# Performance work log

Measured on AMD Instinct MI355X. Metric: run time of the kernel, lower is better.

## Reference

```python
import jax, jax.numpy as jnp
import numpy as np

N = 10000        # num_nodes
D = 256          # num_attrs
AVG_DEG = 32
K = N // 2       # known nodes
ALPHA = 0.5
BETA = 0.5


def setup_inputs() -> dict:
    rng = np.random.default_rng(0)
    # random graph -> symmetric adjacency (duplicate edges coalesce by summation,
    # matching torch_geometric coalescing of edge weights)
    src = rng.integers(0, N, size=N * AVG_DEG)
    dst = rng.integers(0, N, size=N * AVG_DEG)
    A = np.zeros((N, N), dtype=np.float32)
    np.add.at(A, (src, dst), 1.0)
    np.add.at(A, (dst, src), 1.0)
    # symmetric normalized Laplacian: L = I - D^{-1/2} A D^{-1/2}
    deg = A.sum(axis=1)
    dinv = np.where(deg > 0, 1.0 / np.sqrt(np.maximum(deg, 1e-12)), 0.0).astype(np.float32)
    L = np.eye(N, dtype=np.float32) - (dinv[:, None] * A * dinv[None, :])

    raw_x = rng.standard_normal((N, D)).astype(np.float32)
    know = np.sort(rng.choice(N, size=K, replace=False)).astype(np.int64)
    mean = raw_x[know].mean(axis=0)                 # is_binary=False path
    out_k_init = (raw_x[know] - mean).astype(np.float32)  # std = 1
    x = np.zeros((N, D), dtype=np.float32)
    x[know] = raw_x[know]                           # nn.Parameter init

    theta = np.float32((1.0 - 1.0 / N) * (1.0 / ALPHA - 1.0))
    eta = np.float32((1.0 / BETA - 1.0) / ALPHA)
    return {
        "x": jnp.asarray(x),
        "L": jnp.asarray(L),
        "mean": jnp.asarray(mean),
        "out_k_init": jnp.asarray(out_k_init),
        "know_mask": jnp.asarray(know),
        "theta": jnp.asarray(theta),
        "eta": jnp.asarray(eta),
    }


def reference(x, L, mean, out_k_init, know_mask, theta, eta):
    n = x.shape[0]
    xn = x - mean  # std = 1
    # dirichlet loss: sum_f x_f^T L x_f == sum(xn * (L @ xn))
    dirichlet = jnp.sum(xn * (L @ xn))
    # avg_L = n/(n-1) I - 1/(n-1) 11^T  ->  quadratic form in closed form
    col = xn.sum(axis=0)  # [D]
    avg = (n / (n - 1)) * jnp.sum(xn * xn) - (1.0 / (n - 1)) * jnp.sum(col * col)
    # MSE with reduction='sum'
    recon = jnp.sum((xn[know_mask] - out_k_init) ** 2)
    return -(dirichlet + eta * recon + theta * avg)
```

## Files before the change

kernel.cpp:

```cpp
#include <hip/hip_runtime.h>


#define NN    10000
#define DD    256
#define PREPB 157
#define RECB  256
#define SBLK  1250
#define QCAP  2048

typedef float  f32x4 __attribute__((ext_vector_type(4)));
typedef short  s16x8 __attribute__((ext_vector_type(8)));
typedef short  s16x4 __attribute__((ext_vector_type(4)));

__device__ __forceinline__ unsigned short f2bf(float f) {
    union { float f; unsigned u; } c; c.f = f;
    unsigned u = c.u;
    u += 0x7fffu + ((u >> 16) & 1u);
    return (unsigned short)(u >> 16);
}
__device__ __forceinline__ float bfr(unsigned short h) {
    union { unsigned u; float f; } c; c.u = ((unsigned)h) << 16; return c.f;
}

__global__ __launch_bounds__(256) void prep_kernel(const float* __restrict__ x,
                                                   const float* __restrict__ mean,
                                                   const float* __restrict__ oki,
                                                   const int* __restrict__ know,
                                                   int K,
                                                   unsigned short* __restrict__ xnR,
                                                   float* __restrict__ csbuf,
                                                   float* __restrict__ ssbuf,
                                                   float* __restrict__ rbuf) {
    __shared__ __align__(16) unsigned short xs[64][264];
    __shared__ float red[8];
    const int t  = threadIdx.x;
    const int bb = blockIdx.x;
    if (bb < PREPB) {
        const int i0 = bb * 64;
        float ss = 0.f;
#pragma unroll
        for (int p = 0; p < 16; ++p) {
            const int li  = p * 256 + t;
            const int row = li >> 6;
            const int c4  = li & 63;
            const int gi  = i0 + row;
            f32x4 v = {0.f, 0.f, 0.f, 0.f};
            if (gi < NN) {
                const f32x4 xv = *(const f32x4*)(x + (size_t)gi * DD + c4 * 4);
                const f32x4 mv = *(const f32x4*)(mean + c4 * 4);
                v[0] = xv[0] - mv[0]; v[1] = xv[1] - mv[1];
                v[2] = xv[2] - mv[2]; v[3] = xv[3] - mv[3];
                ss += v[0]*v[0] + v[1]*v[1] + v[2]*v[2] + v[3]*v[3];
            }
            unsigned short h[4];
            h[0] = f2bf(v[0]); h[1] = f2bf(v[1]); h[2] = f2bf(v[2]); h[3] = f2bf(v[3]);
            *(s16x4*)&xs[row][c4 * 4] = *(const s16x4*)h;
        }
#pragma unroll
        for (int off = 32; off > 0; off >>= 1) ss += __shfl_xor(ss, off);
        if ((t & 63) == 0) red[t >> 6] = ss;
        __syncthreads();
        if (t == 0) ssbuf[bb] = red[0] + red[1] + red[2] + red[3];
        float css = 0.f;
        for (int ii = 0; ii < 64; ++ii) css += bfr(xs[ii][t]);
        csbuf[(size_t)bb * 256 + t] = css;
#pragma unroll
        for (int p = 0; p < 8; ++p) {
            const int row  = p * 8 + (t >> 5);
            const int colb = (t & 31) * 8;
            const int i = i0 + row;
            if (i < NN)
                *(s16x8*)(xnR + (size_t)i * DD + colb) = *(const s16x8*)&xs[row][colb];
        }
    } else {
        const int rb = bb - PREPB;
        const int w  = t >> 6, l = t & 63;
        const f32x4 mv = *(const f32x4*)(mean + l * 4);
        float s = 0.f;
        for (int r = rb * 4 + w; r < K; r += RECB * 4) {
            const int idx = know[r];
            const f32x4 xv = *(const f32x4*)(x   + (size_t)idx * DD + l * 4);
            const f32x4 ov = *(const f32x4*)(oki + (size_t)r   * DD + l * 4);
            const float d0 = xv[0] - mv[0] - ov[0];
            const float d1 = xv[1] - mv[1] - ov[1];
            const float d2 = xv[2] - mv[2] - ov[2];
            const float d3 = xv[3] - mv[3] - ov[3];
            s += d0*d0 + d1*d1 + d2*d2 + d3*d3;
        }
#pragma unroll
        for (int off = 32; off > 0; off >>= 1) s += __shfl_xor(s, off);
        if (l == 0) red[4 + w] = s;
        __syncthreads();
        if (t == 0) rbuf[rb] = red[4] + red[5] + red[6] + red[7];
    }
}

__global__ __launch_bounds__(256) void sdot_kernel(const float* __restrict__ L,
                                                   const unsigned short* __restrict__ xnR,
                                                   float* __restrict__ part) {
    __shared__ unsigned qidx[QCAP];
    __shared__ float    qval[QCAP];
    __shared__ __align__(16) unsigned short irw[8][264];
    __shared__ unsigned qcnt;
    __shared__ float red[4];
    const int t = threadIdx.x;
    const int b = blockIdx.x;
    const int r0 = 8 * b;
    if (t == 0) qcnt = 0;
    {
        const int sr = t >> 5, sc = (t & 31) * 8;
        *(s16x8*)&irw[sr][sc] = *(const s16x8*)(xnR + (size_t)(r0 + sr) * DD + sc);
    }
    __syncthreads();

    const int lenA = (NN - r0 + 15) >> 4;
    const int lenB = (NN - r0 - 4 + 15) >> 4;
    const int pre1 = lenA;            const int pre2 = 2 * lenA;
    const int pre3 = 3 * lenA;        const int pre4 = 4 * lenA;
    const int pre5 = pre4 + lenB;     const int pre6 = pre4 + 2 * lenB;
    const int pre7 = pre4 + 3 * lenB;
    const int ntot = pre4 + 4 * lenB;

#define DECODE(g_)                                                             \
    int rr_ = 0, base_ = 0;                                                    \
    if ((g_) >= pre1) { rr_ = 1; base_ = pre1; }                               \
    if ((g_) >= pre2) { rr_ = 2; base_ = pre2; }                               \
    if ((g_) >= pre3) { rr_ = 3; base_ = pre3; }                               \
    if ((g_) >= pre4) { rr_ = 4; base_ = pre4; }                               \
    if ((g_) >= pre5) { rr_ = 5; base_ = pre5; }                               \
    if ((g_) >= pre6) { rr_ = 6; base_ = pre6; }                               \
    if ((g_) >= pre7) { rr_ = 7; base_ = pre7; }                               \
    const int i_ = r0 + rr_;                                                   \
    const int c_ = (i_ & ~3) + (((g_) - base_) << 4);

#define ISSUE(V0_, V1_, V2_, V3_, g_) {                                        \
    if ((g_) < ntot) {                                                         \
        DECODE(g_)                                                             \
        const float* p_ = L + (size_t)i_ * NN + c_;                            \
        if (c_ + 16 <= NN) {                                                   \
            V0_ = *(const f32x4*)p_;        V1_ = *(const f32x4*)(p_ + 4);     \
            V2_ = *(const f32x4*)(p_ + 8);  V3_ = *(const f32x4*)(p_ + 12);    \
        } else {                                                               \
            _Pragma("unroll") for (int e_ = 0; e_ < 4; ++e_) {                 \
                V0_[e_] = (c_ + e_      < NN) ? p_[e_]      : 0.f;             \
                V1_[e_] = (c_ + e_ + 4  < NN) ? p_[e_ + 4]  : 0.f;             \
                V2_[e_] = (c_ + e_ + 8  < NN) ? p_[e_ + 8]  : 0.f;             \
                V3_[e_] = (c_ + e_ + 12 < NN) ? p_[e_ + 12] : 0.f;             \
            } } } }

#define PROC(V0_, V1_, V2_, V3_, g_) {                                         \
    if ((g_) < ntot) {                                                         \
        unsigned orv_ = 0u;                                                    \
        _Pragma("unroll") for (int e_ = 0; e_ < 4; ++e_)                       \
            orv_ |= __float_as_uint(V0_[e_]) | __float_as_uint(V1_[e_])        \
                  | __float_as_uint(V2_[e_]) | __float_as_uint(V3_[e_]);       \
        if (orv_ != 0u) {                                                      \
            DECODE(g_)                                                         \
            _Pragma("unroll") for (int e_ = 0; e_ < 16; ++e_) {                \
                const float v_ = (e_ < 4) ? V0_[e_] : (e_ < 8) ? V1_[e_ - 4]   \
                               : (e_ < 12) ? V2_[e_ - 8] : V3_[e_ - 12];       \
                const int j_ = c_ + e_;                                        \
                if (v_ != 0.f && j_ >= i_ && j_ < NN) {                        \
                    const unsigned s_ = atomicAdd(&qcnt, 1u);                  \
                    if (s_ < QCAP) {                                           \
                        qidx[s_] = ((unsigned)rr_ << 14) | (unsigned)j_;       \
                        qval[s_] = (j_ == i_) ? v_ : 2.f * v_;                 \
                    } } } } } }

    f32x4 A0, A1, A2, A3, B0, B1, B2, B3, C0, C1, C2, C3;
    int g = t;
    ISSUE(A0, A1, A2, A3, g)
    ISSUE(B0, B1, B2, B3, g + 256)
    ISSUE(C0, C1, C2, C3, g + 512)
    while (g < ntot) {
        PROC (A0, A1, A2, A3, g)
        ISSUE(A0, A1, A2, A3, g + 768)
        PROC (B0, B1, B2, B3, g + 256)
        ISSUE(B0, B1, B2, B3, g + 1024)
        PROC (C0, C1, C2, C3, g + 512)
        ISSUE(C0, C1, C2, C3, g + 1280)
        g += 768;
    }
#undef ISSUE
#undef PROC
#undef DECODE
    __syncthreads();
    const unsigned cnt = (qcnt < QCAP) ? qcnt : QCAP;

    const int grp = t >> 3;
    const int ln  = t & 7;
    const int cb  = ln * 32;
    float acc = 0.f;
    for (unsigned e = grp; e < cnt; e += 64) {
        const unsigned eB   = e + 32;
        const bool     hasB = (eB < cnt);
        const unsigned pkA = qidx[e];
        const unsigned pkB = hasB ? qidx[eB] : pkA;
        const int rrA = (int)(pkA >> 14), jA = (int)(pkA & 16383u);
        const int rrB = (int)(pkB >> 14), jB = (int)(pkB & 16383u);
        const unsigned short* pjA = xnR + (size_t)jA * DD + cb;
        const unsigned short* pjB = xnR + (size_t)jB * DD + cb;
        float dA = 0.f, dB = 0.f;
        {
            const s16x8 ja0 = *(const s16x8*)pjA,        ja1 = *(const s16x8*)(pjA + 8);
            const s16x8 jb0 = *(const s16x8*)pjB,        jb1 = *(const s16x8*)(pjB + 8);
            const s16x8 ia0 = *(const s16x8*)&irw[rrA][cb];
            const s16x8 ia1 = *(const s16x8*)&irw[rrA][cb + 8];
            const s16x8 ib0 = *(const s16x8*)&irw[rrB][cb];
            const s16x8 ib1 = *(const s16x8*)&irw[rrB][cb + 8];
#pragma unroll
            for (int k = 0; k < 8; ++k) {
                dA += bfr((unsigned short)ia0[k]) * bfr((unsigned short)ja0[k]);
                dB += bfr((unsigned short)ib0[k]) * bfr((unsigned short)jb0[k]);
            }
#pragma unroll
            for (int k = 0; k < 8; ++k) {
                dA += bfr((unsigned short)ia1[k]) * bfr((unsigned short)ja1[k]);
                dB += bfr((unsigned short)ib1[k]) * bfr((unsigned short)jb1[k]);
            }
        }
        {
            const s16x8 ja2 = *(const s16x8*)(pjA + 16), ja3 = *(const s16x8*)(pjA + 24);
            const s16x8 jb2 = *(const s16x8*)(pjB + 16), jb3 = *(const s16x8*)(pjB + 24);
            const s16x8 ia2 = *(const s16x8*)&irw[rrA][cb + 16];
            const s16x8 ia3 = *(const s16x8*)&irw[rrA][cb + 24];
            const s16x8 ib2 = *(const s16x8*)&irw[rrB][cb + 16];
            const s16x8 ib3 = *(const s16x8*)&irw[rrB][cb + 24];
#pragma unroll
            for (int k = 0; k < 8; ++k) {
                dA += bfr((unsigned short)ia2[k]) * bfr((unsigned short)ja2[k]);
                dB += bfr((unsigned short)ib2[k]) * bfr((unsigned short)jb2[k]);
            }
#pragma unroll
            for (int k = 0; k < 8; ++k) {
                dA += bfr((unsigned short)ia3[k]) * bfr((unsigned short)ja3[k]);
                dB += bfr((unsigned short)ib3[k]) * bfr((unsigned short)jb3[k]);
            }
        }
#pragma unroll
        for (int off = 1; off < 8; off <<= 1) {
            dA += __shfl_xor(dA, off);
            dB += __shfl_xor(dB, off);
        }
        if (ln == 0) {
            acc += qval[e] * dA;
            if (hasB) acc += qval[eB] * dB;
        }
    }
#pragma unroll
    for (int off = 32; off > 0; off >>= 1) acc += __shfl_xor(acc, off);
    if ((t & 63) == 0) red[t >> 6] = acc;
    __syncthreads();
    if (t == 0) part[b] = red[0] + red[1] + red[2] + red[3];
}

__global__ __launch_bounds__(256) void fin_kernel(const float* __restrict__ part,
                                                  const float* __restrict__ csbuf,
                                                  const float* __restrict__ ssbuf,
                                                  const float* __restrict__ rbuf,
                                                  const float* __restrict__ theta,
                                                  const float* __restrict__ eta,
                                                  float* __restrict__ out) {
    __shared__ float red[4][4];
    const int t = threadIdx.x;
    float sp = 0.f;
    for (int i = t; i < SBLK; i += 256) sp += part[i];
    float cs = 0.f;
    for (int bb = 0; bb < PREPB; ++bb) cs += csbuf[(size_t)bb * 256 + t];
    float c2 = cs * cs;
    float ssv = (t < PREPB) ? ssbuf[t] : 0.f;
    float rv  = rbuf[t];
#pragma unroll
    for (int off = 32; off > 0; off >>= 1) {
        sp  += __shfl_xor(sp, off);
        c2  += __shfl_xor(c2, off);
        ssv += __shfl_xor(ssv, off);
        rv  += __shfl_xor(rv, off);
    }
    if ((t & 63) == 0) {
        red[t >> 6][0] = sp; red[t >> 6][1] = c2;
        red[t >> 6][2] = ssv; red[t >> 6][3] = rv;
    }
    __syncthreads();
    if (t == 0) {
        float dir = 0.f, colsq = 0.f, ss = 0.f, rec = 0.f;
#pragma unroll
        for (int w = 0; w < 4; ++w) {
            dir += red[w][0]; colsq += red[w][1];
            ss  += red[w][2]; rec   += red[w][3];
        }
        const float n = (float)NN;
        const float avg = (n / (n - 1.f)) * ss - colsq / (n - 1.f);
        out[0] = -(dir + eta[0] * rec + theta[0] * avg);
    }
}

extern "C" void kernel_launch(void* const* d_in, const int* in_sizes, int n_in,
                              void* d_out, int out_size, void* d_ws, size_t ws_size,
                              hipStream_t stream) {
    const float* x     = (const float*)d_in[0];
    const float* L     = (const float*)d_in[1];
    const float* mean  = (const float*)d_in[2];
    const float* oki   = (const float*)d_in[3];
    const int*   know  = (const int*)d_in[4];
    const float* theta = (const float*)d_in[5];
    const float* eta   = (const float*)d_in[6];
    float* out = (float*)d_out;

    char* ws = (char*)d_ws;
    unsigned short* xnR = (unsigned short*)ws;
    float* part  = (float*)(ws + 6 * 1024 * 1024);
    float* csbuf = (float*)(ws + 7 * 1024 * 1024);
    float* ssbuf = (float*)(ws + 8 * 1024 * 1024);
    float* rbuf  = (float*)(ws + 8 * 1024 * 1024 + 4096);
    const int K = in_sizes[4];

    hipLaunchKernelGGL(prep_kernel, dim3(PREPB + RECB), dim3(256), 0, stream,
                       x, mean, oki, know, K, xnR, csbuf, ssbuf, rbuf);
    hipLaunchKernelGGL(sdot_kernel, dim3(SBLK), dim3(256), 0, stream, L, xnR, part);
    hipLaunchKernelGGL(fin_kernel,  dim3(1),    dim3(256), 0, stream,
                       part, csbuf, ssbuf, rbuf, theta, eta, out);
}
```

Measured before the change: 83.63 us.

## Fuse prep and sparse-dot kernels, drop bf16 copy, pair rows for balance

Merges the prep and sparse-dot passes into one launch, so the sparse-dot blocks no longer wait for a bf16 copy of the centered features. They read fp32 x directly and subtract the mean on the fly. Each block now pairs four rows from the top with four rows from the bottom of the upper triangle, which evens out per-block scan length. This removes a kernel boundary and a write/read of the intermediate, at the cost of reading fp32 gathers (twice the bytes of bf16) in the dot-product phase.

```diff
diff --git a/kernel.cpp b/kernel.cpp
--- a/kernel.cpp
+++ b/kernel.cpp
@@ -7,119 +7,66 @@
 #define RECB  256
 #define SBLK  1250
 #define QCAP  2048
+#define NBLK  (SBLK + PREPB + RECB)
 
 typedef float  f32x4 __attribute__((ext_vector_type(4)));
-typedef short  s16x8 __attribute__((ext_vector_type(8)));
-typedef short  s16x4 __attribute__((ext_vector_type(4)));
-
-__device__ __forceinline__ unsigned short f2bf(float f) {
-    union { float f; unsigned u; } c; c.f = f;
-    unsigned u = c.u;
-    u += 0x7fffu + ((u >> 16) & 1u);
-    return (unsigned short)(u >> 16);
-}
-__device__ __forceinline__ float bfr(unsigned short h) {
-    union { unsigned u; float f; } c; c.u = ((unsigned)h) << 16; return c.f;
-}
-
-__global__ __launch_bounds__(256) void prep_kernel(const float* __restrict__ x,
+
+__global__ __launch_bounds__(256) void mega_kernel(const float* __restrict__ L,
+                                                   const float* __restrict__ x,
                                                    const float* __restrict__ mean,
                                                    const float* __restrict__ oki,
                                                    const int* __restrict__ know,
                                                    int K,
-                                                   unsigned short* __restrict__ xnR,
+                                                   float* __restrict__ part,
                                                    float* __restrict__ csbuf,
                                                    float* __restrict__ ssbuf,
                                                    float* __restrict__ rbuf) {
-    __shared__ __align__(16) unsigned short xs[64][264];
-    __shared__ float red[8];
+    __shared__ __align__(16) char smem[26688];
+    unsigned* qidx = (unsigned*)smem;
+    float*    qval = (float*)(smem + 8192);
+    char*     irw  = smem + 16384;
+    float*    red  = (float*)(smem + 26624);
+    unsigned* qcnt = (unsigned*)(smem + 26640);
+    float*    xsf  = (float*)smem;
+#define XSF(r_, c_) xsf[(r_) * 68 + (c_)]
+#define IRW(rr_, ln_) (irw + (rr_) * 1280 + (ln_) * 80)
+
     const int t  = threadIdx.x;
     const int bb = blockIdx.x;
-    if (bb < PREPB) {
-        const int i0 = bb * 64;
-        float ss = 0.f;
-#pragma unroll
-        for (int p = 0; p < 16; ++p) {
-            const int li  = p * 256 + t;
-            const int row = li >> 6;
-            const int c4  = li & 63;
-            const int gi  = i0 + row;
-            f32x4 v = {0.f, 0.f, 0.f, 0.f};
-            if (gi < NN) {
-                const f32x4 xv = *(const f32x4*)(x + (size_t)gi * DD + c4 * 4);
-                const f32x4 mv = *(const f32x4*)(mean + c4 * 4);
-                v[0] = xv[0] - mv[0]; v[1] = xv[1] - mv[1];
-                v[2] = xv[2] - mv[2]; v[3] = xv[3] - mv[3];
-                ss += v[0]*v[0] + v[1]*v[1] + v[2]*v[2] + v[3]*v[3];
-            }
-            unsigned short h[4];
-            h[0] = f2bf(v[0]); h[1] = f2bf(v[1]); h[2] = f2bf(v[2]); h[3] = f2bf(v[3]);
-            *(s16x4*)&xs[row][c4 * 4] = *(const s16x4*)h;
-        }
-#pragma unroll
-        for (int off = 32; off > 0; off >>= 1) ss += __shfl_xor(ss, off);
-        if ((t & 63) == 0) red[t >> 6] = ss;
-        __syncthreads();
-        if (t == 0) ssbuf[bb] = red[0] + red[1] + red[2] + red[3];
-        float css = 0.f;
-        for (int ii = 0; ii < 64; ++ii) css += bfr(xs[ii][t]);
-        csbuf[(size_t)bb * 256 + t] = css;
-#pragma unroll
-        for (int p = 0; p < 8; ++p) {
-            const int row  = p * 8 + (t >> 5);
-            const int colb = (t & 31) * 8;
-            const int i = i0 + row;
-            if (i < NN)
-                *(s16x8*)(xnR + (size_t)i * DD + colb) = *(const s16x8*)&xs[row][colb];
-        }
-    } else {
-        const int rb = bb - PREPB;
-        const int w  = t >> 6, l = t & 63;
-        const f32x4 mv = *(const f32x4*)(mean + l * 4);
-        float s = 0.f;
-        for (int r = rb * 4 + w; r < K; r += RECB * 4) {
-            const int idx = know[r];
-            const f32x4 xv = *(const f32x4*)(x   + (size_t)idx * DD + l * 4);
-            const f32x4 ov = *(const f32x4*)(oki + (size_t)r   * DD + l * 4);
-            const float d0 = xv[0] - mv[0] - ov[0];
-            const float d1 = xv[1] - mv[1] - ov[1];
-            const float d2 = xv[2] - mv[2] - ov[2];
-            const float d3 = xv[3] - mv[3] - ov[3];
-            s += d0*d0 + d1*d1 + d2*d2 + d3*d3;
-        }
-#pragma unroll
-        for (int off = 32; off > 0; off >>= 1) s += __shfl_xor(s, off);
-        if (l == 0) red[4 + w] = s;
-        __syncthreads();
-        if (t == 0) rbuf[rb] = red[4] + red[5] + red[6] + red[7];
-    }
-}
-
-__global__ __launch_bounds__(256) void sdot_kernel(const float* __restrict__ L,
-                                                   const unsigned short* __restrict__ xnR,
-                                                   float* __restrict__ part) {
-    __shared__ unsigned qidx[QCAP];
-    __shared__ float    qval[QCAP];
-    __shared__ __align__(16) unsigned short irw[8][264];
-    __shared__ unsigned qcnt;
-    __shared__ float red[4];
-    const int t = threadIdx.x;
-    const int b = blockIdx.x;
-    const int r0 = 8 * b;
-    if (t == 0) qcnt = 0;
-    {
-        const int sr = t >> 5, sc = (t & 31) * 8;
-        *(s16x8*)&irw[sr][sc] = *(const s16x8*)(xnR + (size_t)(r0 + sr) * DD + sc);
-    }
-    __syncthreads();
-
-    const int lenA = (NN - r0 + 15) >> 4;
-    const int lenB = (NN - r0 - 4 + 15) >> 4;
-    const int pre1 = lenA;            const int pre2 = 2 * lenA;
-    const int pre3 = 3 * lenA;        const int pre4 = 4 * lenA;
-    const int pre5 = pre4 + lenB;     const int pre6 = pre4 + 2 * lenB;
-    const int pre7 = pre4 + 3 * lenB;
-    const int ntot = pre4 + 4 * lenB;
+
+    if (bb < SBLK) {
+        const int b   = bb;
+        const int ibt = 4 * b;
+        const int ibb = NN - 8 - 4 * b;
+        if (t == 0) *qcnt = 0;
+        {
+            const int sr = t >> 5, q = t & 31;
+            const int si = (sr < 4) ? (ibt + sr) : (ibb + sr);
+            const int c8 = q * 8;
+            const f32x4 xv0 = *(const f32x4*)(x + (size_t)si * DD + c8);
+            const f32x4 xv1 = *(const f32x4*)(x + (size_t)si * DD + c8 + 4);
+            const f32x4 mv0 = *(const f32x4*)(mean + c8);
+            const f32x4 mv1 = *(const f32x4*)(mean + c8 + 4);
+            f32x4 a, c;
+            a[0]=xv0[0]-mv0[0]; a[1]=xv0[1]-mv0[1]; a[2]=xv0[2]-mv0[2]; a[3]=xv0[3]-mv0[3];
+            c[0]=xv1[0]-mv1[0]; c[1]=xv1[1]-mv1[1]; c[2]=xv1[2]-mv1[2]; c[3]=xv1[3]-mv1[3];
+            char* dst = IRW(sr, q >> 1) + (q & 1) * 32;
+            *(f32x4*)dst        = a;
+            *(f32x4*)(dst + 16) = c;
+        }
+        __syncthreads();
+
+#define ROWLEN(i_) ((NN - ((i_) & ~3) + 15) >> 4)
+        const int l0 = ROWLEN(ibt);     const int l1 = ROWLEN(ibt + 1);
+        const int l2 = ROWLEN(ibt + 2); const int l3 = ROWLEN(ibt + 3);
+        const int l4 = ROWLEN(ibb + 4); const int l5 = ROWLEN(ibb + 5);
+        const int l6 = ROWLEN(ibb + 6);
+        const int pre1 = l0;        const int pre2 = pre1 + l1;
+        const int pre3 = pre2 + l2; const int pre4 = pre3 + l3;
+        const int pre5 = pre4 + l4; const int pre6 = pre5 + l5;
+        const int pre7 = pre6 + l6;
+        const int ntot = pre7 + ROWLEN(ibb + 7);
+#undef ROWLEN
 
 #define DECODE(g_)                                                             \
     int rr_ = 0, base_ = 0;                                                    \
@@ -130,7 +77,7 @@
     if ((g_) >= pre5) { rr_ = 5; base_ = pre5; }                               \
     if ((g_) >= pre6) { rr_ = 6; base_ = pre6; }                               \
     if ((g_) >= pre7) { rr_ = 7; base_ = pre7; }                               \
-    const int i_ = r0 + rr_;                                                   \
+    const int i_ = (rr_ < 4) ? (ibt + rr_) : (ibb + rr_);                      \
     const int c_ = (i_ & ~3) + (((g_) - base_) << 4);
 
 #define ISSUE(V0_, V1_, V2_, V3_, g_) {                                        \
@@ -161,97 +108,147 @@
                                : (e_ < 12) ? V2_[e_ - 8] : V3_[e_ - 12];       \
                 const int j_ = c_ + e_;                                        \
                 if (v_ != 0.f && j_ >= i_ && j_ < NN) {                        \
-                    const unsigned s_ = atomicAdd(&qcnt, 1u);                  \
+                    const unsigned s_ = atomicAdd(qcnt, 1u);                   \
                     if (s_ < QCAP) {                                           \
                         qidx[s_] = ((unsigned)rr_ << 14) | (unsigned)j_;       \
                         qval[s_] = (j_ == i_) ? v_ : 2.f * v_;                 \
                     } } } } } }
 
-    f32x4 A0, A1, A2, A3, B0, B1, B2, B3, C0, C1, C2, C3;
-    int g = t;
-    ISSUE(A0, A1, A2, A3, g)
-    ISSUE(B0, B1, B2, B3, g + 256)
-    ISSUE(C0, C1, C2, C3, g + 512)
-    while (g < ntot) {
-        PROC (A0, A1, A2, A3, g)
-        ISSUE(A0, A1, A2, A3, g + 768)
-        PROC (B0, B1, B2, B3, g + 256)
-        ISSUE(B0, B1, B2, B3, g + 1024)
-        PROC (C0, C1, C2, C3, g + 512)
-        ISSUE(C0, C1, C2, C3, g + 1280)
-        g += 768;
-    }
+        f32x4 A0, A1, A2, A3, B0, B1, B2, B3, C0, C1, C2, C3;
+        int g = t;
+        ISSUE(A0, A1, A2, A3, g)
+        ISSUE(B0, B1, B2, B3, g + 256)
+        ISSUE(C0, C1, C2, C3, g + 512)
+        while (g < ntot) {
+            PROC (A0, A1, A2, A3, g)
+            ISSUE(A0, A1, A2, A3, g + 768)
+            PROC (B0, B1, B2, B3, g + 256)
+            ISSUE(B0, B1, B2, B3, g + 1024)
+            PROC (C0, C1, C2, C3, g + 512)
+            ISSUE(C0, C1, C2, C3, g + 1280)
+            g += 768;
+        }
 #undef ISSUE
 #undef PROC
 #undef DECODE
-    __syncthreads();
-    const unsigned cnt = (qcnt < QCAP) ? qcnt : QCAP;
-
-    const int grp = t >> 3;
-    const int ln  = t & 7;
-    const int cb  = ln * 32;
-    float acc = 0.f;
-    for (unsigned e = grp; e < cnt; e += 64) {
-        const unsigned eB   = e + 32;
-        const bool     hasB = (eB < cnt);
-        const unsigned pkA = qidx[e];
-        const unsigned pkB = hasB ? qidx[eB] : pkA;
-        const int rrA = (int)(pkA >> 14), jA = (int)(pkA & 16383u);
-        const int rrB = (int)(pkB >> 14), jB = (int)(pkB & 16383u);
-        const unsigned short* pjA = xnR + (size_t)jA * DD + cb;
-        const unsigned short* pjB = xnR + (size_t)jB * DD + cb;
-        float dA = 0.f, dB = 0.f;
-        {
-            const s16x8 ja0 = *(const s16x8*)pjA,        ja1 = *(const s16x8*)(pjA + 8);
-            const s16x8 jb0 = *(const s16x8*)pjB,        jb1 = *(const s16x8*)(pjB + 8);
-            const s16x8 ia0 = *(const s16x8*)&irw[rrA][cb];
-            const s16x8 ia1 = *(const s16x8*)&irw[rrA][cb + 8];
-            const s16x8 ib0 = *(const s16x8*)&irw[rrB][cb];
-            const s16x8 ib1 = *(const s16x8*)&irw[rrB][cb + 8];
-#pragma unroll
-            for (int k = 0; k < 8; ++k) {
-                dA += bfr((unsigned short)ia0[k]) * bfr((unsigned short)ja0[k]);
-                dB += bfr((unsigned short)ib0[k]) * bfr((unsigned short)jb0[k]);
+        __syncthreads();
+        const unsigned cnt = (*qcnt < QCAP) ? *qcnt : QCAP;
+
+        const int grp = t >> 4;
+        const int ln  = t & 15;
+        const int cb  = ln * 16;
+        const f32x4 m0 = *(const f32x4*)(mean + cb);
+        const f32x4 m1 = *(const f32x4*)(mean + cb + 4);
+        const f32x4 m2 = *(const f32x4*)(mean + cb + 8);
+        const f32x4 m3 = *(const f32x4*)(mean + cb + 12);
+        float acc = 0.f;
+        for (unsigned e = grp; e < cnt; e += 32) {
+            const unsigned eB   = e + 16;
+            const bool     hasB = (eB < cnt);
+            const unsigned pkA = qidx[e];
+            const unsigned pkB = hasB ? qidx[eB] : pkA;
+            const int rrA = (int)(pkA >> 14), jA = (int)(pkA & 16383u);
+            const int rrB = (int)(pkB >> 14), jB = (int)(pkB & 16383u);
+            const float* pjA = x + (size_t)jA * DD + cb;
+            const float* pjB = x + (size_t)jB * DD + cb;
+            const f32x4 ja0 = *(const f32x4*)pjA;
+            const f32x4 ja1 = *(const f32x4*)(pjA + 4);
+            const f32x4 ja2 = *(const f32x4*)(pjA + 8);
+            const f32x4 ja3 = *(const f32x4*)(pjA + 12);
+            const f32x4 jb0 = *(const f32x4*)pjB;
+            const f32x4 jb1 = *(const f32x4*)(pjB + 4);
+            const f32x4 jb2 = *(const f32x4*)(pjB + 8);
+            const f32x4 jb3 = *(const f32x4*)(pjB + 12);
+            const char* iA = IRW(rrA, ln);
+            const char* iB = IRW(rrB, ln);
+            const f32x4 ia0 = *(const f32x4*)iA;
+            const f32x4 ia1 = *(const f32x4*)(iA + 16);
+            const f32x4 ia2 = *(const f32x4*)(iA + 32);
+            const f32x4 ia3 = *(const f32x4*)(iA + 48);
+            const f32x4 ib0 = *(const f32x4*)iB;
+            const f32x4 ib1 = *(const f32x4*)(iB + 16);
+            const f32x4 ib2 = *(const f32x4*)(iB + 32);
+            const f32x4 ib3 = *(const f32x4*)(iB + 48);
+            float dA = 0.f, dB = 0.f;
+#pragma unroll
+            for (int k = 0; k < 4; ++k) {
+                dA += (ja0[k] - m0[k]) * ia0[k] + (ja1[k] - m1[k]) * ia1[k]
+                    + (ja2[k] - m2[k]) * ia2[k] + (ja3[k] - m3[k]) * ia3[k];
+                dB += (jb0[k] - m0[k]) * ib0[k] + (jb1[k] - m1[k]) * ib1[k]
+                    + (jb2[k] - m2[k]) * ib2[k] + (jb3[k] - m3[k]) * ib3[k];
             }
 #pragma unroll
-            for (int k = 0; k < 8; ++k) {
-                dA += bfr((unsigned short)ia1[k]) * bfr((unsigned short)ja1[k]);
-                dB += bfr((unsigned short)ib1[k]) * bfr((unsigned short)jb1[k]);
+            for (int off = 1; off < 16; off <<= 1) {
+                dA += __shfl_xor(dA, off);
+                dB += __shfl_xor(dB, off);
             }
-        }
-        {
-            const s16x8 ja2 = *(const s16x8*)(pjA + 16), ja3 = *(const s16x8*)(pjA + 24);
-            const s16x8 jb2 = *(const s16x8*)(pjB + 16), jb3 = *(const s16x8*)(pjB + 24);
-            const s16x8 ia2 = *(const s16x8*)&irw[rrA][cb + 16];
-            const s16x8 ia3 = *(const s16x8*)&irw[rrA][cb + 24];
-            const s16x8 ib2 = *(const s16x8*)&irw[rrB][cb + 16];
-            const s16x8 ib3 = *(const s16x8*)&irw[rrB][cb + 24];
-#pragma unroll
-            for (int k = 0; k < 8; ++k) {
-                dA += bfr((unsigned short)ia2[k]) * bfr((unsigned short)ja2[k]);
-                dB += bfr((unsigned short)ib2[k]) * bfr((unsigned short)jb2[k]);
+            if (ln == 0) {
+                acc += qval[e] * dA;
+                if (hasB) acc += qval[eB] * dB;
             }
-#pragma unroll
-            for (int k = 0; k < 8; ++k) {
-                dA += bfr((unsigned short)ia3[k]) * bfr((unsigned short)ja3[k]);
-                dB += bfr((unsigned short)ib3[k]) * bfr((unsigned short)jb3[k]);
+        }
+#pragma unroll
+        for (int off = 32; off > 0; off >>= 1) acc += __shfl_xor(acc, off);
+        if ((t & 63) == 0) red[t >> 6] = acc;
+        __syncthreads();
+        if (t == 0) part[b] = red[0] + red[1] + red[2] + red[3];
+
+    } else if (bb < SBLK + PREPB) {
+        const int pb = bb - SBLK;
+        const int i0 = pb * 64;
+        float ss = 0.f;
+#pragma unroll
+        for (int p = 0; p < 16; ++p) {
+            const int li  = p * 256 + t;
+            const int row = li >> 6;
+            const int c4  = li & 63;
+            const int gi  = i0 + row;
+            f32x4 v = {0.f, 0.f, 0.f, 0.f};
+            if (gi < NN) {
+                const f32x4 xv = *(const f32x4*)(x + (size_t)gi * DD + c4 * 4);
+                const f32x4 mv = *(const f32x4*)(mean + c4 * 4);
+                v[0] = xv[0] - mv[0]; v[1] = xv[1] - mv[1];
+                v[2] = xv[2] - mv[2]; v[3] = xv[3] - mv[3];
+                ss += v[0]*v[0] + v[1]*v[1] + v[2]*v[2] + v[3]*v[3];
             }
-        }
-#pragma unroll
-        for (int off = 1; off < 8; off <<= 1) {
-            dA += __shfl_xor(dA, off);
-            dB += __shfl_xor(dB, off);
-        }
-        if (ln == 0) {
-            acc += qval[e] * dA;
-            if (hasB) acc += qval[eB] * dB;
-        }
+            *(f32x4*)&XSF(row, c4 * 4) = v;
+        }
+#pragma unroll
+        for (int off = 32; off > 0; off >>= 1) ss += __shfl_xor(ss, off);
+        __syncthreads();
+        float css = 0.f;
+        for (int ii = 0; ii < 64; ++ii) css += XSF(ii, t);
+        csbuf[(size_t)pb * 256 + t] = css;
+        if (t == 0) { float* r4 = (float*)&XSF(0, 0); (void)r4; }
+        __syncthreads();
+        if ((t & 63) == 0) xsf[t >> 6] = ss;
+        __syncthreads();
+        if (t == 0) ssbuf[pb] = xsf[0] + xsf[1] + xsf[2] + xsf[3];
+
+    } else {
+        const int rb = bb - SBLK - PREPB;
+        const int w  = t >> 6, l = t & 63;
+        const f32x4 mv = *(const f32x4*)(mean + l * 4);
+        float s = 0.f;
+        for (int r = rb * 4 + w; r < K; r += RECB * 4) {
+            const int idx = know[r];
+            const f32x4 xv = *(const f32x4*)(x   + (size_t)idx * DD + l * 4);
+            const f32x4 ov = *(const f32x4*)(oki + (size_t)r   * DD + l * 4);
+            const float d0 = xv[0] - mv[0] - ov[0];
+            const float d1 = xv[1] - mv[1] - ov[1];
+            const float d2 = xv[2] - mv[2] - ov[2];
+            const float d3 = xv[3] - mv[3] - ov[3];
+            s += d0*d0 + d1*d1 + d2*d2 + d3*d3;
+        }
+#pragma unroll
+        for (int off = 32; off > 0; off >>= 1) s += __shfl_xor(s, off);
+        float* r8 = (float*)smem;
+        if (l == 0) r8[w] = s;
+        __syncthreads();
+        if (t == 0) rbuf[rb] = r8[0] + r8[1] + r8[2] + r8[3];
     }
-#pragma unroll
-    for (int off = 32; off > 0; off >>= 1) acc += __shfl_xor(acc, off);
-    if ((t & 63) == 0) red[t >> 6] = acc;
-    __syncthreads();
-    if (t == 0) part[b] = red[0] + red[1] + red[2] + red[3];
+#undef XSF
+#undef IRW
 }
 
 __global__ __launch_bounds__(256) void fin_kernel(const float* __restrict__ part,
@@ -308,16 +305,14 @@
     float* out = (float*)d_out;
 
     char* ws = (char*)d_ws;
-    unsigned short* xnR = (unsigned short*)ws;
-    float* part  = (float*)(ws + 6 * 1024 * 1024);
-    float* csbuf = (float*)(ws + 7 * 1024 * 1024);
-    float* ssbuf = (float*)(ws + 8 * 1024 * 1024);
-    float* rbuf  = (float*)(ws + 8 * 1024 * 1024 + 4096);
+    float* part  = (float*)ws;
+    float* csbuf = (float*)(ws + 1 * 1024 * 1024);
+    float* ssbuf = (float*)(ws + 2 * 1024 * 1024);
+    float* rbuf  = (float*)(ws + 2 * 1024 * 1024 + 4096);
     const int K = in_sizes[4];
 
-    hipLaunchKernelGGL(prep_kernel, dim3(PREPB + RECB), dim3(256), 0, stream,
-                       x, mean, oki, know, K, xnR, csbuf, ssbuf, rbuf);
-    hipLaunchKernelGGL(sdot_kernel, dim3(SBLK), dim3(256), 0, stream, L, xnR, part);
+    hipLaunchKernelGGL(mega_kernel, dim3(NBLK), dim3(256), 0, stream,
+                       L, x, mean, oki, know, K, part, csbuf, ssbuf, rbuf);
     hipLaunchKernelGGL(fin_kernel,  dim3(1),    dim3(256), 0, stream,
                        part, csbuf, ssbuf, rbuf, theta, eta, out);
 }
```

Result: slower. 86.35 us (+3.2%).

## Balance triangular row pairing and move reconstruction loss into sdot kernel

Applied to the files above, without the earlier changes.

Each sdot block now takes four rows from the top and four from the bottom of L, so the upper-triangle work per block is roughly equal rather than shrinking with block index. The reconstruction MSE blocks move from the prep kernel into the sdot launch, and prep is split into smaller 32-row blocks so it runs across more blocks. The aim is to remove tail imbalance in the main streaming kernel and shorten the prep launch on the critical path. In exchange there is extra index arithmetic, and fin now reduces ssbuf with a loop because there are more prep blocks.

```diff
diff --git a/kernel.cpp b/kernel.cpp
--- a/kernel.cpp
+++ b/kernel.cpp
@@ -3,7 +3,7 @@
 
 #define NN    10000
 #define DD    256
-#define PREPB 157
+#define PREPB 313
 #define RECB  256
 #define SBLK  1250
 #define QCAP  2048
@@ -24,56 +24,70 @@
 
 __global__ __launch_bounds__(256) void prep_kernel(const float* __restrict__ x,
                                                    const float* __restrict__ mean,
+                                                   unsigned short* __restrict__ xnR,
+                                                   float* __restrict__ csbuf,
+                                                   float* __restrict__ ssbuf) {
+    __shared__ __align__(16) unsigned short xs[32][264];
+    __shared__ float red[4];
+    const int t  = threadIdx.x;
+    const int bb = blockIdx.x;
+    const int i0 = bb * 32;
+    float ss = 0.f;
+#pragma unroll
+    for (int p = 0; p < 8; ++p) {
+        const int li  = p * 256 + t;
+        const int row = li >> 6;
+        const int c4  = li & 63;
+        const int gi  = i0 + row;
+        f32x4 v = {0.f, 0.f, 0.f, 0.f};
+        if (gi < NN) {
+            const f32x4 xv = *(const f32x4*)(x + (size_t)gi * DD + c4 * 4);
+            const f32x4 mv = *(const f32x4*)(mean + c4 * 4);
+            v[0] = xv[0] - mv[0]; v[1] = xv[1] - mv[1];
+            v[2] = xv[2] - mv[2]; v[3] = xv[3] - mv[3];
+            ss += v[0]*v[0] + v[1]*v[1] + v[2]*v[2] + v[3]*v[3];
+        }
+        unsigned short h[4];
+        h[0] = f2bf(v[0]); h[1] = f2bf(v[1]); h[2] = f2bf(v[2]); h[3] = f2bf(v[3]);
+        *(s16x4*)&xs[row][c4 * 4] = *(const s16x4*)h;
+    }
+#pragma unroll
+    for (int off = 32; off > 0; off >>= 1) ss += __shfl_xor(ss, off);
+    if ((t & 63) == 0) red[t >> 6] = ss;
+    __syncthreads();
+    if (t == 0) ssbuf[bb] = red[0] + red[1] + red[2] + red[3];
+    float css = 0.f;
+    for (int ii = 0; ii < 32; ++ii) css += bfr(xs[ii][t]);
+    csbuf[(size_t)bb * 256 + t] = css;
+#pragma unroll
+    for (int p = 0; p < 4; ++p) {
+        const int row  = p * 8 + (t >> 5);
+        const int colb = (t & 31) * 8;
+        const int i = i0 + row;
+        if (i < NN)
+            *(s16x8*)(xnR + (size_t)i * DD + colb) = *(const s16x8*)&xs[row][colb];
+    }
+}
+
+__global__ __launch_bounds__(256) void sdot_kernel(const float* __restrict__ L,
+                                                   const float* __restrict__ x,
+                                                   const float* __restrict__ mean,
                                                    const float* __restrict__ oki,
                                                    const int* __restrict__ know,
                                                    int K,
-                                                   unsigned short* __restrict__ xnR,
-                                                   float* __restrict__ csbuf,
-                                                   float* __restrict__ ssbuf,
+                                                   const unsigned short* __restrict__ xnR,
+                                                   float* __restrict__ part,
                                                    float* __restrict__ rbuf) {
-    __shared__ __align__(16) unsigned short xs[64][264];
-    __shared__ float red[8];
+    __shared__ unsigned qidx[QCAP];
+    __shared__ float    qval[QCAP];
+    __shared__ __align__(16) unsigned short irw[8][264];
+    __shared__ unsigned qcnt;
+    __shared__ float red[4];
     const int t  = threadIdx.x;
     const int bb = blockIdx.x;
-    if (bb < PREPB) {
-        const int i0 = bb * 64;
-        float ss = 0.f;
-#pragma unroll
-        for (int p = 0; p < 16; ++p) {
-            const int li  = p * 256 + t;
-            const int row = li >> 6;
-            const int c4  = li & 63;
-            const int gi  = i0 + row;
-            f32x4 v = {0.f, 0.f, 0.f, 0.f};
-            if (gi < NN) {
-                const f32x4 xv = *(const f32x4*)(x + (size_t)gi * DD + c4 * 4);
-                const f32x4 mv = *(const f32x4*)(mean + c4 * 4);
-                v[0] = xv[0] - mv[0]; v[1] = xv[1] - mv[1];
-                v[2] = xv[2] - mv[2]; v[3] = xv[3] - mv[3];
-                ss += v[0]*v[0] + v[1]*v[1] + v[2]*v[2] + v[3]*v[3];
-            }
-            unsigned short h[4];
-            h[0] = f2bf(v[0]); h[1] = f2bf(v[1]); h[2] = f2bf(v[2]); h[3] = f2bf(v[3]);
-            *(s16x4*)&xs[row][c4 * 4] = *(const s16x4*)h;
-        }
-#pragma unroll
-        for (int off = 32; off > 0; off >>= 1) ss += __shfl_xor(ss, off);
-        if ((t & 63) == 0) red[t >> 6] = ss;
-        __syncthreads();
-        if (t == 0) ssbuf[bb] = red[0] + red[1] + red[2] + red[3];
-        float css = 0.f;
-        for (int ii = 0; ii < 64; ++ii) css += bfr(xs[ii][t]);
-        csbuf[(size_t)bb * 256 + t] = css;
-#pragma unroll
-        for (int p = 0; p < 8; ++p) {
-            const int row  = p * 8 + (t >> 5);
-            const int colb = (t & 31) * 8;
-            const int i = i0 + row;
-            if (i < NN)
-                *(s16x8*)(xnR + (size_t)i * DD + colb) = *(const s16x8*)&xs[row][colb];
-        }
-    } else {
-        const int rb = bb - PREPB;
+
+    if (bb >= SBLK) {
+        const int rb = bb - SBLK;
         const int w  = t >> 6, l = t & 63;
         const f32x4 mv = *(const f32x4*)(mean + l * 4);
         float s = 0.f;
@@ -89,37 +103,34 @@
         }
 #pragma unroll
         for (int off = 32; off > 0; off >>= 1) s += __shfl_xor(s, off);
-        if (l == 0) red[4 + w] = s;
+        if (l == 0) red[w] = s;
         __syncthreads();
-        if (t == 0) rbuf[rb] = red[4] + red[5] + red[6] + red[7];
-    }
-}
-
-__global__ __launch_bounds__(256) void sdot_kernel(const float* __restrict__ L,
-                                                   const unsigned short* __restrict__ xnR,
-                                                   float* __restrict__ part) {
-    __shared__ unsigned qidx[QCAP];
-    __shared__ float    qval[QCAP];
-    __shared__ __align__(16) unsigned short irw[8][264];
-    __shared__ unsigned qcnt;
-    __shared__ float red[4];
-    const int t = threadIdx.x;
-    const int b = blockIdx.x;
-    const int r0 = 8 * b;
+        if (t == 0) rbuf[rb] = red[0] + red[1] + red[2] + red[3];
+        return;
+    }
+
+    const int b   = bb;
+    const int ibt = 4 * b;
+    const int ibb = NN - 8 - 4 * b;
     if (t == 0) qcnt = 0;
     {
         const int sr = t >> 5, sc = (t & 31) * 8;
-        *(s16x8*)&irw[sr][sc] = *(const s16x8*)(xnR + (size_t)(r0 + sr) * DD + sc);
-    }
-    __syncthreads();
-
-    const int lenA = (NN - r0 + 15) >> 4;
-    const int lenB = (NN - r0 - 4 + 15) >> 4;
-    const int pre1 = lenA;            const int pre2 = 2 * lenA;
-    const int pre3 = 3 * lenA;        const int pre4 = 4 * lenA;
-    const int pre5 = pre4 + lenB;     const int pre6 = pre4 + 2 * lenB;
-    const int pre7 = pre4 + 3 * lenB;
-    const int ntot = pre4 + 4 * lenB;
+        const int si = (sr < 4) ? (ibt + sr) : (ibb + sr);
+        *(s16x8*)&irw[sr][sc] = *(const s16x8*)(xnR + (size_t)si * DD + sc);
+    }
+    __syncthreads();
+
+#define ROWLEN(i_) ((NN - (((i_) >> 2) << 2) + 15) >> 4)
+    const int l0 = ROWLEN(ibt);     const int l1 = ROWLEN(ibt + 1);
+    const int l2 = ROWLEN(ibt + 2); const int l3 = ROWLEN(ibt + 3);
+    const int l4 = ROWLEN(ibb + 4); const int l5 = ROWLEN(ibb + 5);
+    const int l6 = ROWLEN(ibb + 6);
+    const int pre1 = l0;        const int pre2 = pre1 + l1;
+    const int pre3 = pre2 + l2; const int pre4 = pre3 + l3;
+    const int pre5 = pre4 + l4; const int pre6 = pre5 + l5;
+    const int pre7 = pre6 + l6;
+    const int ntot = pre7 + ROWLEN(ibb + 7);
+#undef ROWLEN
 
 #define DECODE(g_)                                                             \
     int rr_ = 0, base_ = 0;                                                    \
@@ -130,8 +141,8 @@
     if ((g_) >= pre5) { rr_ = 5; base_ = pre5; }                               \
     if ((g_) >= pre6) { rr_ = 6; base_ = pre6; }                               \
     if ((g_) >= pre7) { rr_ = 7; base_ = pre7; }                               \
-    const int i_ = r0 + rr_;                                                   \
-    const int c_ = (i_ & ~3) + (((g_) - base_) << 4);
+    const int i_ = (rr_ < 4) ? (ibt + rr_) : (ibb + rr_);                      \
+    const int c_ = (((i_) >> 2) << 2) + (((g_) - base_) << 4);
 
 #define ISSUE(V0_, V1_, V2_, V3_, g_) {                                        \
     if ((g_) < ntot) {                                                         \
@@ -268,7 +279,8 @@
     float cs = 0.f;
     for (int bb = 0; bb < PREPB; ++bb) cs += csbuf[(size_t)bb * 256 + t];
     float c2 = cs * cs;
-    float ssv = (t < PREPB) ? ssbuf[t] : 0.f;
+    float ssv = 0.f;
+    for (int i = t; i < PREPB; i += 256) ssv += ssbuf[i];
     float rv  = rbuf[t];
 #pragma unroll
     for (int off = 32; off > 0; off >>= 1) {
@@ -315,9 +327,10 @@
     float* rbuf  = (float*)(ws + 8 * 1024 * 1024 + 4096);
     const int K = in_sizes[4];
 
-    hipLaunchKernelGGL(prep_kernel, dim3(PREPB + RECB), dim3(256), 0, stream,
-                       x, mean, oki, know, K, xnR, csbuf, ssbuf, rbuf);
-    hipLaunchKernelGGL(sdot_kernel, dim3(SBLK), dim3(256), 0, stream, L, xnR, part);
-    hipLaunchKernelGGL(fin_kernel,  dim3(1),    dim3(256), 0, stream,
+    hipLaunchKernelGGL(prep_kernel, dim3(PREPB),        dim3(256), 0, stream,
+                       x, mean, xnR, csbuf, ssbuf);
+    hipLaunchKernelGGL(sdot_kernel, dim3(SBLK + RECB),  dim3(256), 0, stream,
+                       L, x, mean, oki, know, K, xnR, part, rbuf);
+    hipLaunchKernelGGL(fin_kernel,  dim3(1),            dim3(256), 0, stream,
                        part, csbuf, ssbuf, rbuf, theta, eta, out);
 }
```

Result: slower. 90.63 us (+8.4%).
